# Optimization experiments

Measured on AMD Instinct MI355X. Metric: run time of the kernel, lower is better.

The kernel has to match this reference:

```python
import jax, jax.numpy as jnp
import numpy as np

MARGIN = 1.0
EPS = 1e-6  # F.pairwise_distance adds eps to the elementwise diff


def setup_inputs() -> dict:
    key = jax.random.key(0)
    k1, k2, k3 = jax.random.split(key, 3)
    N, D = 8192, 64
    anchor_embeddings = jax.random.normal(k1, (N, D), dtype=jnp.float32)
    positive_embeddings = jax.random.normal(k2, (N, D), dtype=jnp.float32)
    labels = jax.random.randint(k3, (N,), 0, 2, dtype=jnp.int64)
    return {
        "anchor_embeddings": anchor_embeddings,
        "positive_embeddings": positive_embeddings,
        "labels": labels,
    }


def _pairwise_dist(a, p):
    # dist[i, j] = ||(a_i + eps) - p_j||_2, matching F.pairwise_distance's
    # norm(x1 - x2 + eps). Computed via the Gram trick to avoid an [N,N,D]
    # intermediate.
    a = a + EPS
    a2 = jnp.sum(a * a, axis=-1)                      # [N]
    p2 = jnp.sum(p * p, axis=-1)                      # [N]
    sq = a2[:, None] + p2[None, :] - 2.0 * (a @ p.T)  # [N, N]
    return jnp.sqrt(jnp.maximum(sq, 1e-12))


def reference(anchor_embeddings, positive_embeddings, labels):
    N = anchor_embeddings.shape[0]
    dist = _pairwise_dist(anchor_embeddings, positive_embeddings)  # [N, N]
    pos_dist = jnp.diagonal(dist)                                  # [N], d(a_i, p_i)
    hinge = jax.nn.relu(pos_dist[:, None] - dist + MARGIN)         # [N, N]
    # pair (i, j) contributes iff labels[i] == 1 and i != j
    row_mask = (labels == 1)[:, None]
    offdiag = ~jnp.eye(N, dtype=bool)
    mask = (row_mask & offdiag).astype(hinge.dtype)
    count = jnp.sum(mask)
    total = jnp.sum(hinge * mask)
    return jnp.where(count > 0, total / jnp.maximum(count, 1.0), 0.0)
```

## Files before the change

kernel.cpp:

```cpp
#include <hip/hip_runtime.h>
#include <hip/hip_bf16.h>

#define NROWS 8192
#define DDIM 64
#define MARGIN_F 1.0f
#define EPS_F 1e-6f


typedef __attribute__((ext_vector_type(8))) short bf16x8;
typedef __attribute__((ext_vector_type(4))) float f32x4;

__global__ __launch_bounds__(256) void
prep_kernel(const float* __restrict__ A, const float* __restrict__ P,
            __hip_bfloat16* __restrict__ Abf, __hip_bfloat16* __restrict__ Pbf,
            float* __restrict__ a2g, float* __restrict__ pdg,
            float* __restrict__ p2g) {
    int row  = blockIdx.x * 4 + (threadIdx.x >> 6);
    int lane = threadIdx.x & 63;
    float av = A[row * DDIM + lane] + EPS_F;
    float pv = P[row * DDIM + lane];
    Abf[row * DDIM + lane] = __float2bfloat16(av);
    Pbf[row * DDIM + lane] = __float2bfloat16(pv);
    float va2 = av * av;
    float vp2 = pv * pv;
    float vap = av * pv;
    #pragma unroll
    for (int off = 32; off; off >>= 1) {
        va2 += __shfl_xor(va2, off);
        vp2 += __shfl_xor(vp2, off);
        vap += __shfl_xor(vap, off);
    }
    if (lane == 0) {
        a2g[row] = va2;
        p2g[row] = vp2;
        float sq = fmaxf(va2 + vp2 - 2.0f * vap, 1e-12f);
        pdg[row] = sqrtf(sq) + MARGIN_F;
    }
}

__global__ __launch_bounds__(256) void
compact_kernel(const int* __restrict__ labels, int* __restrict__ sel,
               int* __restrict__ cnt, float* __restrict__ total) {
    __shared__ int scan[256];
    int t = threadIdx.x;
    int lc = 0;
    #pragma unroll
    for (int i = 0; i < 32; ++i)
        lc += (labels[t * 32 + i] == 1) ? 1 : 0;
    scan[t] = lc;
    __syncthreads();
    #pragma unroll
    for (int off = 1; off < 256; off <<= 1) {
        int v = (t >= off) ? scan[t - off] : 0;
        __syncthreads();
        if (t >= off) scan[t] += v;
        __syncthreads();
    }
    int o = scan[t] - lc;
    for (int i = 0; i < 32; ++i) {
        int r = t * 32 + i;
        if (labels[r] == 1) sel[o++] = r;
    }
    if (t == 255) *cnt = scan[255];
    if (t == 0)   *total = 0.0f;
}

#define LDS_STRIDE 72

__global__ __launch_bounds__(256) void
main_kernel(const __hip_bfloat16* __restrict__ Abf, const __hip_bfloat16* __restrict__ Pbf,
            const float* __restrict__ a2g, const float* __restrict__ pdg,
            const float* __restrict__ p2g, const int* __restrict__ sel,
            const int* __restrict__ cnt, float* __restrict__ total) {
    __shared__ __align__(16) unsigned short As[128 * LDS_STRIDE];
    __shared__ __align__(16) unsigned short Ps2[128 * LDS_STRIDE];
    __shared__ float sA2[128], sPd[128], sP2[128];
    __shared__ int   sGi[128];
    __shared__ float wsum[4];

    int M = *cnt;
    int row0 = blockIdx.y * 128;
    int col0 = blockIdx.x * 128;
    if (row0 >= M) return;

    int t = threadIdx.x;

    if (t < 128) {
        int gi = sel[min(row0 + t, M - 1)];
        sGi[t] = gi;
        sA2[t] = a2g[gi];
        sPd[t] = pdg[gi];
        sP2[t] = p2g[col0 + t];
    }
    __syncthreads();

    const float4* Asrc = (const float4*)Abf;
    const float4* Psrc = (const float4*)Pbf;
    #pragma unroll
    for (int i = 0; i < 4; ++i) {
        int c  = t + i * 256;
        int r  = c >> 3;
        int kc = c & 7;
        int ar = sGi[r];
        *(float4*)&As[r * LDS_STRIDE + kc * 8]  = Asrc[ar * 8 + kc];
        *(float4*)&Ps2[r * LDS_STRIDE + kc * 8] = Psrc[(col0 + r) * 8 + kc];
    }
    __syncthreads();

    int wid  = t >> 6;
    int lane = t & 63;
    int wm = (wid >> 1) * 64;
    int wn = (wid & 1) * 64;
    int lm   = lane & 15;
    int quad = lane >> 4;

    f32x4 acc[4][4] = {};
    #pragma unroll
    for (int s = 0; s < 2; ++s) {
        bf16x8 af[4], bfr[4];
        #pragma unroll
        for (int a = 0; a < 4; ++a)
            af[a] = *(const bf16x8*)&As[(wm + a * 16 + lm) * LDS_STRIDE + s * 32 + quad * 8];
        #pragma unroll
        for (int b = 0; b < 4; ++b)
            bfr[b] = *(const bf16x8*)&Ps2[(wn + b * 16 + lm) * LDS_STRIDE + s * 32 + quad * 8];
        #pragma unroll
        for (int a = 0; a < 4; ++a)
            #pragma unroll
            for (int b = 0; b < 4; ++b)
                acc[a][b] = __builtin_amdgcn_mfma_f32_16x16x32_bf16(af[a], bfr[b], acc[a][b], 0, 0, 0);
    }

    float bsum = 0.0f;
    #pragma unroll
    for (int a = 0; a < 4; ++a) {
        #pragma unroll
        for (int r = 0; r < 4; ++r) {
            int il = wm + a * 16 + quad * 4 + r;
            bool valid = (row0 + il) < M;
            float ra2 = sA2[il];
            float rpd = sPd[il];
            int   gi  = sGi[il];
            #pragma unroll
            for (int b = 0; b < 4; ++b) {
                int jl = wn + b * 16 + lm;
                int j  = col0 + jl;
                float sq = fmaxf(ra2 + sP2[jl] - 2.0f * acc[a][b][r], 1e-12f);
                float h  = rpd - sqrtf(sq);
                if (valid && (gi != j) && (h > 0.0f)) bsum += h;
            }
        }
    }

    #pragma unroll
    for (int off = 32; off; off >>= 1) bsum += __shfl_xor(bsum, off);
    if (lane == 0) wsum[wid] = bsum;
    __syncthreads();
    if (t == 0) atomicAdd(total, wsum[0] + wsum[1] + wsum[2] + wsum[3]);
}

__global__ void finalize_kernel(const int* __restrict__ cnt,
                                const float* __restrict__ total,
                                float* __restrict__ out) {
    int M = *cnt;
    float c = (float)M * (float)(NROWS - 1);
    out[0] = (M > 0) ? (*total) / c : 0.0f;
}

extern "C" void kernel_launch(void* const* d_in, const int* in_sizes, int n_in,
                              void* d_out, int out_size, void* d_ws, size_t ws_size,
                              hipStream_t stream) {
    const float* A      = (const float*)d_in[0];
    const float* P      = (const float*)d_in[1];
    const int*   labels = (const int*)d_in[2];
    float* out = (float*)d_out;

    char* ws = (char*)d_ws;
    __hip_bfloat16* Abf = (__hip_bfloat16*)(ws);
    __hip_bfloat16* Pbf = (__hip_bfloat16*)(ws + (1 << 20));
    float* a2g   = (float*)(ws + (2 << 20));
    float* pdg   = (float*)(ws + (2 << 20) + 32768);
    float* p2g   = (float*)(ws + (2 << 20) + 65536);
    int*   sel   = (int*)(ws + (2 << 20) + 98304);
    int*   cnt   = (int*)(ws + (2 << 20) + 131072);
    float* total = (float*)(ws + (2 << 20) + 131076);

    prep_kernel<<<dim3(NROWS / 4), dim3(256), 0, stream>>>(A, P, Abf, Pbf, a2g, pdg, p2g);
    compact_kernel<<<dim3(1), dim3(256), 0, stream>>>(labels, sel, cnt, total);

    dim3 grid(NROWS / 128, NROWS / 128);
    main_kernel<<<grid, dim3(256), 0, stream>>>(Abf, Pbf, a2g, pdg, p2g, sel, cnt, total);

    finalize_kernel<<<1, 1, 0, stream>>>(cnt, total, out);
}
```

Baseline: 107.4 us.

## Load MFMA fragments directly from global, vectorize prep, replace atomics with partials

Measured after the change: 96.60 us. -10.0%, faster.

```diff
diff --git a/kernel.cpp b/kernel.cpp
--- a/kernel.cpp
+++ b/kernel.cpp
@@ -10,27 +10,38 @@
 typedef __attribute__((ext_vector_type(8))) short bf16x8;
 typedef __attribute__((ext_vector_type(4))) float f32x4;
 
+static __device__ __forceinline__ unsigned short f2bf(float x) {
+    __hip_bfloat16 h = __float2bfloat16(x);
+    return *reinterpret_cast<unsigned short*>(&h);
+}
+
 __global__ __launch_bounds__(256) void
 prep_kernel(const float* __restrict__ A, const float* __restrict__ P,
-            __hip_bfloat16* __restrict__ Abf, __hip_bfloat16* __restrict__ Pbf,
+            unsigned short* __restrict__ Abf, unsigned short* __restrict__ Pbf,
             float* __restrict__ a2g, float* __restrict__ pdg,
             float* __restrict__ p2g) {
-    int row  = blockIdx.x * 4 + (threadIdx.x >> 6);
-    int lane = threadIdx.x & 63;
-    float av = A[row * DDIM + lane] + EPS_F;
-    float pv = P[row * DDIM + lane];
-    Abf[row * DDIM + lane] = __float2bfloat16(av);
-    Pbf[row * DDIM + lane] = __float2bfloat16(pv);
-    float va2 = av * av;
-    float vp2 = pv * pv;
-    float vap = av * pv;
-    #pragma unroll
-    for (int off = 32; off; off >>= 1) {
+    int t   = threadIdx.x;
+    int gid = blockIdx.x * 256 + t;
+    int row = gid >> 4;
+    int c4  = (gid & 15) * 4;
+    float4 a = *(const float4*)&A[row * DDIM + c4];
+    float4 p = *(const float4*)&P[row * DDIM + c4];
+    a.x += EPS_F; a.y += EPS_F; a.z += EPS_F; a.w += EPS_F;
+    ushort4 ab, pb;
+    ab.x = f2bf(a.x); ab.y = f2bf(a.y); ab.z = f2bf(a.z); ab.w = f2bf(a.w);
+    pb.x = f2bf(p.x); pb.y = f2bf(p.y); pb.z = f2bf(p.z); pb.w = f2bf(p.w);
+    *(ushort4*)&Abf[row * DDIM + c4] = ab;
+    *(ushort4*)&Pbf[row * DDIM + c4] = pb;
+    float va2 = a.x*a.x + a.y*a.y + a.z*a.z + a.w*a.w;
+    float vp2 = p.x*p.x + p.y*p.y + p.z*p.z + p.w*p.w;
+    float vap = a.x*p.x + a.y*p.y + a.z*p.z + a.w*p.w;
+    #pragma unroll
+    for (int off = 8; off; off >>= 1) {
         va2 += __shfl_xor(va2, off);
         vp2 += __shfl_xor(vp2, off);
         vap += __shfl_xor(vap, off);
     }
-    if (lane == 0) {
+    if ((t & 15) == 0) {
         a2g[row] = va2;
         p2g[row] = vp2;
         float sq = fmaxf(va2 + vp2 - 2.0f * vap, 1e-12f);
@@ -40,16 +51,21 @@
 
 __global__ __launch_bounds__(256) void
 compact_kernel(const int* __restrict__ labels, int* __restrict__ sel,
-               int* __restrict__ cnt, float* __restrict__ total) {
+               int* __restrict__ cnt) {
+    __shared__ int lab[256 * 33];
     __shared__ int scan[256];
     int t = threadIdx.x;
+    #pragma unroll
+    for (int i = 0; i < 32; ++i) {
+        int j = i * 256 + t;
+        lab[(j >> 5) * 33 + (j & 31)] = labels[j];
+    }
+    __syncthreads();
     int lc = 0;
     #pragma unroll
-    for (int i = 0; i < 32; ++i)
-        lc += (labels[t * 32 + i] == 1) ? 1 : 0;
+    for (int i = 0; i < 32; ++i) lc += (lab[t * 33 + i] == 1) ? 1 : 0;
     scan[t] = lc;
     __syncthreads();
-    #pragma unroll
     for (int off = 1; off < 256; off <<= 1) {
         int v = (t >= off) ? scan[t - off] : 0;
         __syncthreads();
@@ -58,22 +74,16 @@
     }
     int o = scan[t] - lc;
     for (int i = 0; i < 32; ++i) {
-        int r = t * 32 + i;
-        if (labels[r] == 1) sel[o++] = r;
+        if (lab[t * 33 + i] == 1) sel[o++] = t * 32 + i;
     }
     if (t == 255) *cnt = scan[255];
-    if (t == 0)   *total = 0.0f;
-}
-
-#define LDS_STRIDE 72
-
-__global__ __launch_bounds__(256) void
-main_kernel(const __hip_bfloat16* __restrict__ Abf, const __hip_bfloat16* __restrict__ Pbf,
+}
+
+__global__ __launch_bounds__(256) void
+main_kernel(const unsigned short* __restrict__ Abf, const unsigned short* __restrict__ Pbf,
             const float* __restrict__ a2g, const float* __restrict__ pdg,
             const float* __restrict__ p2g, const int* __restrict__ sel,
-            const int* __restrict__ cnt, float* __restrict__ total) {
-    __shared__ __align__(16) unsigned short As[128 * LDS_STRIDE];
-    __shared__ __align__(16) unsigned short Ps2[128 * LDS_STRIDE];
+            const int* __restrict__ cnt, float* __restrict__ partial) {
     __shared__ float sA2[128], sPd[128], sP2[128];
     __shared__ int   sGi[128];
     __shared__ float wsum[4];
@@ -81,9 +91,9 @@
     int M = *cnt;
     int row0 = blockIdx.y * 128;
     int col0 = blockIdx.x * 128;
-    if (row0 >= M) return;
-
+    int bid  = blockIdx.y * 64 + blockIdx.x;
     int t = threadIdx.x;
+    if (row0 >= M) { if (t == 0) partial[bid] = 0.0f; return; }
 
     if (t < 128) {
         int gi = sel[min(row0 + t, M - 1)];
@@ -94,19 +104,6 @@
     }
     __syncthreads();
 
-    const float4* Asrc = (const float4*)Abf;
-    const float4* Psrc = (const float4*)Pbf;
-    #pragma unroll
-    for (int i = 0; i < 4; ++i) {
-        int c  = t + i * 256;
-        int r  = c >> 3;
-        int kc = c & 7;
-        int ar = sGi[r];
-        *(float4*)&As[r * LDS_STRIDE + kc * 8]  = Asrc[ar * 8 + kc];
-        *(float4*)&Ps2[r * LDS_STRIDE + kc * 8] = Psrc[(col0 + r) * 8 + kc];
-    }
-    __syncthreads();
-
     int wid  = t >> 6;
     int lane = t & 63;
     int wm = (wid >> 1) * 64;
@@ -114,22 +111,28 @@
     int lm   = lane & 15;
     int quad = lane >> 4;
 
+    bf16x8 af[2][4], bg[2][4];
+    #pragma unroll
+    for (int a = 0; a < 4; ++a) {
+        const unsigned short* pa = Abf + (size_t)sGi[wm + a * 16 + lm] * DDIM + quad * 8;
+        af[0][a] = *(const bf16x8*)pa;
+        af[1][a] = *(const bf16x8*)(pa + 32);
+    }
+    #pragma unroll
+    for (int b = 0; b < 4; ++b) {
+        const unsigned short* pb = Pbf + (size_t)(col0 + wn + b * 16 + lm) * DDIM + quad * 8;
+        bg[0][b] = *(const bf16x8*)pb;
+        bg[1][b] = *(const bf16x8*)(pb + 32);
+    }
+
     f32x4 acc[4][4] = {};
     #pragma unroll
-    for (int s = 0; s < 2; ++s) {
-        bf16x8 af[4], bfr[4];
-        #pragma unroll
-        for (int a = 0; a < 4; ++a)
-            af[a] = *(const bf16x8*)&As[(wm + a * 16 + lm) * LDS_STRIDE + s * 32 + quad * 8];
-        #pragma unroll
-        for (int b = 0; b < 4; ++b)
-            bfr[b] = *(const bf16x8*)&Ps2[(wn + b * 16 + lm) * LDS_STRIDE + s * 32 + quad * 8];
+    for (int s = 0; s < 2; ++s)
         #pragma unroll
         for (int a = 0; a < 4; ++a)
             #pragma unroll
             for (int b = 0; b < 4; ++b)
-                acc[a][b] = __builtin_amdgcn_mfma_f32_16x16x32_bf16(af[a], bfr[b], acc[a][b], 0, 0, 0);
-    }
+                acc[a][b] = __builtin_amdgcn_mfma_f32_16x16x32_bf16(af[s][a], bg[s][b], acc[a][b], 0, 0, 0);
 
     float bsum = 0.0f;
     #pragma unroll
@@ -156,15 +159,31 @@
     for (int off = 32; off; off >>= 1) bsum += __shfl_xor(bsum, off);
     if (lane == 0) wsum[wid] = bsum;
     __syncthreads();
-    if (t == 0) atomicAdd(total, wsum[0] + wsum[1] + wsum[2] + wsum[3]);
-}
-
-__global__ void finalize_kernel(const int* __restrict__ cnt,
-                                const float* __restrict__ total,
-                                float* __restrict__ out) {
-    int M = *cnt;
-    float c = (float)M * (float)(NROWS - 1);
-    out[0] = (M > 0) ? (*total) / c : 0.0f;
+    if (t == 0) partial[bid] = wsum[0] + wsum[1] + wsum[2] + wsum[3];
+}
+
+__global__ __launch_bounds__(256) void
+finalize_kernel(const int* __restrict__ cnt, const float* __restrict__ partial,
+                float* __restrict__ out) {
+    __shared__ float wsum[4];
+    int t = threadIdx.x;
+    const float4* p4 = (const float4*)partial;
+    float s = 0.0f;
+    #pragma unroll
+    for (int i = 0; i < 4; ++i) {
+        float4 v = p4[i * 256 + t];
+        s += v.x + v.y + v.z + v.w;
+    }
+    #pragma unroll
+    for (int off = 32; off; off >>= 1) s += __shfl_xor(s, off);
+    if ((t & 63) == 0) wsum[t >> 6] = s;
+    __syncthreads();
+    if (t == 0) {
+        int M = *cnt;
+        float tot = wsum[0] + wsum[1] + wsum[2] + wsum[3];
+        float c = (float)M * (float)(NROWS - 1);
+        out[0] = (M > 0) ? tot / c : 0.0f;
+    }
 }
 
 extern "C" void kernel_launch(void* const* d_in, const int* in_sizes, int n_in,
@@ -176,20 +195,20 @@
     float* out = (float*)d_out;
 
     char* ws = (char*)d_ws;
-    __hip_bfloat16* Abf = (__hip_bfloat16*)(ws);
-    __hip_bfloat16* Pbf = (__hip_bfloat16*)(ws + (1 << 20));
-    float* a2g   = (float*)(ws + (2 << 20));
-    float* pdg   = (float*)(ws + (2 << 20) + 32768);
-    float* p2g   = (float*)(ws + (2 << 20) + 65536);
-    int*   sel   = (int*)(ws + (2 << 20) + 98304);
-    int*   cnt   = (int*)(ws + (2 << 20) + 131072);
-    float* total = (float*)(ws + (2 << 20) + 131076);
-
-    prep_kernel<<<dim3(NROWS / 4), dim3(256), 0, stream>>>(A, P, Abf, Pbf, a2g, pdg, p2g);
-    compact_kernel<<<dim3(1), dim3(256), 0, stream>>>(labels, sel, cnt, total);
+    unsigned short* Abf = (unsigned short*)(ws);
+    unsigned short* Pbf = (unsigned short*)(ws + (1 << 20));
+    float* a2g     = (float*)(ws + (2 << 20));
+    float* pdg     = (float*)(ws + (2 << 20) + 32768);
+    float* p2g     = (float*)(ws + (2 << 20) + 65536);
+    int*   sel     = (int*)(ws + (2 << 20) + 98304);
+    int*   cnt     = (int*)(ws + (2 << 20) + 131072);
+    float* partial = (float*)(ws + (2 << 20) + 135168);
+
+    prep_kernel<<<dim3(NROWS * 16 / 256), dim3(256), 0, stream>>>(A, P, Abf, Pbf, a2g, pdg, p2g);
+    compact_kernel<<<dim3(1), dim3(256), 0, stream>>>(labels, sel, cnt);
 
     dim3 grid(NROWS / 128, NROWS / 128);
-    main_kernel<<<grid, dim3(256), 0, stream>>>(Abf, Pbf, a2g, pdg, p2g, sel, cnt, total);
-
-    finalize_kernel<<<1, 1, 0, stream>>>(cnt, total, out);
-}
+    main_kernel<<<grid, dim3(256), 0, stream>>>(Abf, Pbf, a2g, pdg, p2g, sel, cnt, partial);
+
+    finalize_kernel<<<1, dim3(256), 0, stream>>>(cnt, partial, out);
+}
```
